# Performance work log

Hardware: AMD Instinct MI355X
Metric: run time of the kernel (lower is better)

## Reference

```python
import jax, jax.numpy as jnp
import numpy as np

DIM = 1280
HEADS = 16
HD = DIM // HEADS  # 80
NSEG = 8
LSEG = 1024
SEQ = NSEG * LSEG  # 8192


def _rotate_half(x):
    x1, x2 = jnp.split(x, 2, axis=-1)
    return jnp.concatenate([-x2, x1], axis=-1)


def setup_inputs() -> dict:
    key = jax.random.key(0)
    ks = jax.random.split(key, 6)
    hidden_states = jax.random.normal(ks[0], (SEQ, DIM), dtype=jnp.float32)
    # rotary embedding table: per-position angles over head_dim
    inv_freq = 1.0 / (10000.0 ** (np.arange(0, HD, 2, dtype=np.float32) / HD))
    pos = np.arange(SEQ, dtype=np.float32)
    freqs = np.outer(pos, inv_freq)                    # [SEQ, HD/2]
    emb = np.concatenate([freqs, freqs], axis=-1)      # [SEQ, HD]
    cos = jnp.asarray(np.cos(emb), dtype=jnp.float32)
    sin = jnp.asarray(np.sin(emb), dtype=jnp.float32)
    w_scale = 1.0 / np.sqrt(DIM)
    qkv_w = jax.random.normal(ks[1], (DIM, 3 * DIM), dtype=jnp.float32) * w_scale
    qkv_b = jax.random.normal(ks[2], (3 * DIM,), dtype=jnp.float32) * 0.02
    proj_w = jax.random.normal(ks[3], (DIM, DIM), dtype=jnp.float32) * w_scale
    proj_b = jax.random.normal(ks[4], (DIM,), dtype=jnp.float32) * 0.02
    cu_seqlens = jnp.arange(NSEG + 1, dtype=jnp.int32) * LSEG
    return {
        "hidden_states": hidden_states,
        "cos": cos,
        "sin": sin,
        "qkv_w": qkv_w,
        "qkv_b": qkv_b,
        "proj_w": proj_w,
        "proj_b": proj_b,
        "cu_seqlens": cu_seqlens,
    }


def reference(hidden_states, cos, sin, qkv_w, qkv_b, proj_w, proj_b, cu_seqlens):
    S, D = hidden_states.shape
    n_seg = cu_seqlens.shape[0] - 1          # static
    L = S // n_seg                            # equal-length packed segments
    # fused QKV projection: [S, 3D] -> q, k, v each [S, H, hd]
    qkv = hidden_states @ qkv_w + qkv_b
    q, k, v = (t.reshape(S, HEADS, HD) for t in jnp.split(qkv, 3, axis=-1))
    # RoPE (computed in fp32, as in apply_rotary_pos_emb_vision)
    c = cos.astype(jnp.float32)[:, None, :]   # [S, 1, hd]
    s = sin.astype(jnp.float32)[:, None, :]
    qf = q.astype(jnp.float32)
    kf = k.astype(jnp.float32)
    q = (qf * c + _rotate_half(qf) * s).astype(q.dtype)
    k = (kf * c + _rotate_half(kf) * s).astype(k.dtype)
    # block-diagonal varlen attention == independent attention per segment
    qs = q.reshape(n_seg, L, HEADS, HD)
    ks = k.reshape(n_seg, L, HEADS, HD)
    vs = v.reshape(n_seg, L, HEADS, HD)
    scale = HD ** -0.5
    scores = jnp.einsum("nqhd,nkhd->nhqk", qs, ks) * scale
    probs = jax.nn.softmax(scores.astype(jnp.float32), axis=-1).astype(qs.dtype)
    out = jnp.einsum("nhqk,nkhd->nqhd", probs, vs)     # [n, L, H, hd]
    out = out.reshape(S, D)
    return out @ proj_w + proj_b
```

## Files before the change

kernel.cpp:

```cpp
#include <hip/hip_runtime.h>

#define SEQ   8192
#define DIM   1280
#define HEADS 16
#define HD    80
#define LSEG  1024
#define QKVD  3840

typedef unsigned short USHORT;
typedef __attribute__((ext_vector_type(8))) short bf16x8;
typedef __attribute__((ext_vector_type(4))) float f32x4;
typedef __attribute__((ext_vector_type(4))) USHORT u16x4;
typedef __attribute__((ext_vector_type(4))) int i32x4;

#define CSF  0.16129832f

__device__ __forceinline__ USHORT f2bf(float x) {
  unsigned u = __float_as_uint(x);
  u += 0x7fffu + ((u >> 16) & 1u);
  return (USHORT)(u >> 16);
}
__device__ __forceinline__ float bf2f(USHORT b) {
  return __uint_as_float(((unsigned)b) << 16);
}
__device__ __forceinline__ void gload16(const void* g, void* l) {
  __builtin_amdgcn_global_load_lds(
      (const __attribute__((address_space(1))) void*)g,
      (__attribute__((address_space(3))) void*)l, 16, 0, 0);
}
__device__ __forceinline__ unsigned cvtpk(float a, float b) {
  unsigned d;
  asm("v_cvt_pk_bf16_f32 %0, %1, %2" : "=v"(d) : "v"(a), "v"(b));
  return d;
}
#define SB() __builtin_amdgcn_sched_barrier(0)

__global__ __launch_bounds__(256) void prep1(
    const float* __restrict__ hs, USHORT* __restrict__ hsB,
    const float* __restrict__ qkv_w, USHORT* __restrict__ qkvwT,
    const float* __restrict__ proj_w, USHORT* __restrict__ pwT) {
  __shared__ float tb[32][33];
  const int bx = blockIdx.x;
  const int tid = threadIdx.x;
  if (bx < 10240) {
    const int i = bx * 256 + tid;
    const float4 v = reinterpret_cast<const float4*>(hs)[i];
    USHORT* o = hsB + (size_t)i * 4;
    o[0] = f2bf(v.x); o[1] = f2bf(v.y); o[2] = f2bf(v.z); o[3] = f2bf(v.w);
    return;
  }
  const float* W; USHORT* T; int K, N, n0, k0;
  if (bx < 15040) {
    const int b = bx - 10240;
    W = qkv_w; T = qkvwT; K = DIM; N = QKVD;
    n0 = (b % 120) * 32; k0 = (b / 120) * 32;
  } else {
    const int b = bx - 15040;
    W = proj_w; T = pwT; K = DIM; N = DIM;
    n0 = (b % 40) * 32; k0 = (b / 40) * 32;
  }
  const int c = tid & 31, r0 = tid >> 5;
  for (int r = r0; r < 32; r += 8) tb[r][c] = W[(size_t)(k0 + r) * N + n0 + c];
  __syncthreads();
  for (int r = r0; r < 32; r += 8)
    T[(size_t)(n0 + r) * K + k0 + c] = f2bf(tb[c][r]);
}

__global__ __launch_bounds__(256) void prep2(
    USHORT* __restrict__ qkv, const float* __restrict__ cosb,
    const float* __restrict__ sinb, uint4* __restrict__ zb) {
  const int bx = blockIdx.x;
  const int tid = threadIdx.x;
  if (bx < 10240) {
    int idx = bx * 256 + tid;
    const int d4 = (idx % 10) * 4;
    int t = idx / 10;
    const int h = t % HEADS;
    t /= HEADS;
    const int qk = t & 1;
    const int s = t >> 1;
    USHORT* base = qkv + (size_t)s * QKVD + qk * DIM + h * HD;
    const u16x4 x1 = *(const u16x4*)&base[d4];
    const u16x4 x2 = *(const u16x4*)&base[d4 + 40];
    const f32x4 c1 = *(const f32x4*)&cosb[s * HD + d4];
    const f32x4 s1 = *(const f32x4*)&sinb[s * HD + d4];
    const f32x4 c2 = *(const f32x4*)&cosb[s * HD + d4 + 40];
    const f32x4 s2 = *(const f32x4*)&sinb[s * HD + d4 + 40];
    u16x4 o1, o2;
#pragma unroll
    for (int j = 0; j < 4; ++j) {
      const float a = bf2f(x1[j]), b = bf2f(x2[j]);
      o1[j] = f2bf(a * c1[j] - b * s1[j]);
      o2[j] = f2bf(b * c2[j] + a * s2[j]);
    }
    *(u16x4*)&base[d4] = o1;
    *(u16x4*)&base[d4 + 40] = o2;
    return;
  }
  if (tid < 64) zb[tid] = uint4{0u, 0u, 0u, 0u};
}

__global__ __launch_bounds__(512, 2) void mfma_gemm256(
    const USHORT* __restrict__ Ah, const USHORT* __restrict__ Bh,
    const float* __restrict__ bias, USHORT* __restrict__ Cout,
    USHORT* __restrict__ VtGo, int M, int N, int K, int lda) {
  extern __shared__ USHORT sm[];

  const int tid = threadIdx.x;
  const int l = tid & 63;
  const int w = tid >> 6;
  const int fr = l & 15;
  const int g = l >> 4;
  const int nrow = M >> 8;
  const int nwg = nrow * (N >> 8);
  const int orig = blockIdx.x;
  const int wg = (orig & 7) * (nwg >> 3) + (orig >> 3);
  const int row0 = (wg % nrow) << 8;
  const int col0 = (wg / nrow) << 8;
  const int wr = (w >> 2) << 7;
  const int wc = (w & 3) << 6;

  const f32x4 fz = {0.f, 0.f, 0.f, 0.f};
  f32x4 acc[8][4];
#pragma unroll
  for (int m = 0; m < 8; ++m)
#pragma unroll
    for (int n = 0; n < 4; ++n) acc[m][n] = fz;

  const int NT = K >> 6;

  const USHORT* asrc[4];
  const USHORT* bsrc[4];
#pragma unroll
  for (int i = 0; i < 4; ++i) {
    const int u = i * 512 + tid;
    const int row = u >> 3;
    const int c = (u & 7) ^ (row & 7);
    asrc[i] = Ah + (size_t)(row0 + row) * lda + c * 8;
    bsrc[i] = Bh + (size_t)(col0 + row) * K + c * 8;
  }
  auto stage = [&](int b) {
#pragma unroll
    for (int i = 0; i < 4; ++i) {
      USHORT* dst = sm + (i * 512 + (w << 6)) * 8 + b * 16384;
      gload16(asrc[i], dst);
      gload16(bsrc[i], dst + 32768);
    }
  };
  auto advance = [&]() {
#pragma unroll
    for (int i = 0; i < 4; ++i) { asrc[i] += 64; bsrc[i] += 64; }
  };

  const int fb = fr & 7;
  int aOff[2], bOff[2];
#pragma unroll
  for (int ks = 0; ks < 2; ++ks) {
    const int sl = (((ks << 2) + g) ^ fb) << 3;
    aOff[ks] = (wr + fr) * 64 + sl;
    bOff[ks] = 32768 + (wc + fr) * 64 + sl;
  }

  stage(0); advance();
  stage(1); advance();

  for (int t = 0; t < NT; ++t) {
    const int cur = t & 1;
    asm volatile("s_waitcnt vmcnt(8)" ::: "memory");
    SB();
    __builtin_amdgcn_s_barrier();
    SB();
    const int cb = cur << 14;
    bf16x8 ah[2][8], bh[2][4];
#pragma unroll
    for (int m = 0; m < 8; ++m)
      ah[0][m] = *(const bf16x8*)(sm + cb + aOff[0] + m * 1024);
#pragma unroll
    for (int n = 0; n < 4; ++n)
      bh[0][n] = *(const bf16x8*)(sm + cb + bOff[0] + n * 1024);
    SB();
#pragma unroll
    for (int m = 0; m < 8; ++m)
      ah[1][m] = *(const bf16x8*)(sm + cb + aOff[1] + m * 1024);
#pragma unroll
    for (int n = 0; n < 4; ++n)
      bh[1][n] = *(const bf16x8*)(sm + cb + bOff[1] + n * 1024);
    SB();
    asm volatile("s_waitcnt lgkmcnt(12)" ::: "memory");
    SB();
    __builtin_amdgcn_s_setprio(1);
#pragma unroll
    for (int m = 0; m < 8; ++m)
#pragma unroll
      for (int n = 0; n < 4; ++n)
        acc[m][n] = __builtin_amdgcn_mfma_f32_16x16x32_bf16(
            ah[0][m], bh[0][n], acc[m][n], 0, 0, 0);
    __builtin_amdgcn_s_setprio(0);
    SB();
    asm volatile("s_waitcnt lgkmcnt(0)" ::: "memory");
    SB();
    __builtin_amdgcn_s_barrier();
    SB();
    stage(cur);
    if (t < NT - 3) advance();
    SB();
    __builtin_amdgcn_s_setprio(1);
#pragma unroll
    for (int m = 0; m < 8; ++m)
#pragma unroll
      for (int n = 0; n < 4; ++n)
        acc[m][n] = __builtin_amdgcn_mfma_f32_16x16x32_bf16(
            ah[1][m], bh[1][n], acc[m][n], 0, 0, 0);
    __builtin_amdgcn_s_setprio(0);
  }

  asm volatile("s_waitcnt vmcnt(0)" ::: "memory");

  float bv[4];
#pragma unroll
  for (int n = 0; n < 4; ++n) bv[n] = bias[col0 + wc + n * 16 + fr];
#pragma unroll
  for (int m = 0; m < 8; ++m)
#pragma unroll
    for (int n = 0; n < 4; ++n) {
      const int colb = col0 + wc + n * 16;
      const int row = row0 + wr + m * 16 + g * 4;
      if (colb >= 2 * DIM) {
        u16x4 o;
#pragma unroll
        for (int r = 0; r < 4; ++r) o[r] = f2bf(acc[m][n][r] + bv[n]);
        const int rl = row & 63;
        const int sc = (rl & 0x23) | ((rl & 0x10) >> 2) | ((rl & 0x0C) << 1);
        *(u16x4*)&VtGo[(size_t)(colb + fr - 2 * DIM) * SEQ + (row & ~63) + sc] = o;
      } else {
#pragma unroll
        for (int r = 0; r < 4; ++r)
          Cout[(size_t)(row + r) * N + colb + fr] = f2bf(acc[m][n][r] + bv[n]);
      }
    }
}

__global__ __launch_bounds__(256) void mfma_gemm(
    const USHORT* __restrict__ Ah, const USHORT* __restrict__ Bh,
    const float* __restrict__ bias, float* __restrict__ Cout,
    int M, int N, int K, int lda) {
  __shared__ __align__(16) USHORT AhL[2][8192];
  __shared__ __align__(16) USHORT BhL[2][8192];

  const int tid = threadIdx.x;
  const int l = tid & 63;
  const int w = tid >> 6;
  const int nrow = M >> 7;
  const int nwg = nrow * (N >> 7);
  const int orig = blockIdx.x;
  const int wg = (orig & 7) * (nwg >> 3) + (orig >> 3);
  const int row0 = (wg % nrow) << 7;
  const int col0 = (wg / nrow) << 7;
  const int wr = (w >> 1) << 6;
  const int wc = (w & 1) << 6;

  const f32x4 fz = {0.f, 0.f, 0.f, 0.f};
  f32x4 acc[4][4];
#pragma unroll
  for (int m = 0; m < 4; ++m)
#pragma unroll
    for (int n = 0; n < 4; ++n) acc[m][n] = fz;

  const int fr = l & 15;
  const int g = l >> 4;
  const int NT = K >> 6;

  const USHORT* asrc[4];
  const USHORT* bsrc[4];
#pragma unroll
  for (int i = 0; i < 4; ++i) {
    const int u = (w * 4 + i) * 64 + l;
    const int row = u >> 3;
    const int c = (u & 7) ^ (row & 7);
    asrc[i] = Ah + (size_t)(row0 + row) * lda + c * 8;
    bsrc[i] = Bh + (size_t)(col0 + row) * K + c * 8;
  }
  auto stage = [&](int b) {
#pragma unroll
    for (int i = 0; i < 4; ++i) {
      gload16(asrc[i], &AhL[b][(w * 4 + i) * 512]);
      gload16(bsrc[i], &BhL[b][(w * 4 + i) * 512]);
    }
  };
  auto advance = [&]() {
#pragma unroll
    for (int i = 0; i < 4; ++i) { asrc[i] += 64; bsrc[i] += 64; }
  };

  const int fb = fr & 7;
  int aOff[2], bOff[2];
#pragma unroll
  for (int ks = 0; ks < 2; ++ks) {
    const int sl = (((ks << 2) + g) ^ fb) << 3;
    aOff[ks] = (wr + fr) * 64 + sl;
    bOff[ks] = (wc + fr) * 64 + sl;
  }
  const USHORT* AB = &AhL[0][0];
  const USHORT* BB = &BhL[0][0];

  stage(0); advance();
  stage(1); advance();

  for (int t = 0; t < NT; ++t) {
    const int cur = t & 1;
    asm volatile("s_waitcnt vmcnt(8)" ::: "memory");
    SB();
    __builtin_amdgcn_s_barrier();
    SB();
    const int cb = cur << 13;
    bf16x8 ah[2][4], bh[2][4];
#pragma unroll
    for (int m = 0; m < 4; ++m) {
      ah[0][m] = *(const bf16x8*)(AB + cb + aOff[0] + m * 1024);
      bh[0][m] = *(const bf16x8*)(BB + cb + bOff[0] + m * 1024);
    }
    SB();
#pragma unroll
    for (int m = 0; m < 4; ++m) {
      ah[1][m] = *(const bf16x8*)(AB + cb + aOff[1] + m * 1024);
      bh[1][m] = *(const bf16x8*)(BB + cb + bOff[1] + m * 1024);
    }
    SB();
    asm volatile("s_waitcnt lgkmcnt(8)" ::: "memory");
    SB();
    __builtin_amdgcn_s_setprio(1);
#pragma unroll
    for (int m = 0; m < 4; ++m)
#pragma unroll
      for (int n = 0; n < 4; ++n)
        acc[m][n] = __builtin_amdgcn_mfma_f32_16x16x32_bf16(
            ah[0][m], bh[0][n], acc[m][n], 0, 0, 0);
    __builtin_amdgcn_s_setprio(0);
    SB();
    asm volatile("s_waitcnt lgkmcnt(0)" ::: "memory");
    SB();
    __builtin_amdgcn_s_barrier();
    SB();
    stage(cur);
    if (t < NT - 3) advance();
    SB();
    __builtin_amdgcn_s_setprio(1);
#pragma unroll
    for (int m = 0; m < 4; ++m)
#pragma unroll
      for (int n = 0; n < 4; ++n)
        acc[m][n] = __builtin_amdgcn_mfma_f32_16x16x32_bf16(
            ah[1][m], bh[1][n], acc[m][n], 0, 0, 0);
    __builtin_amdgcn_s_setprio(0);
  }

  asm volatile("s_waitcnt vmcnt(0)" ::: "memory");

  float bv[4];
#pragma unroll
  for (int n = 0; n < 4; ++n) bv[n] = bias[col0 + wc + n * 16 + fr];
#pragma unroll
  for (int m = 0; m < 4; ++m)
#pragma unroll
    for (int n = 0; n < 4; ++n)
#pragma unroll
      for (int r = 0; r < 4; ++r) {
        const float v = acc[m][n][r] + bv[n];
        const int row = row0 + wr + m * 16 + (l >> 4) * 4 + r;
        const int col = col0 + wc + n * 16 + fr;
        Cout[(size_t)row * N + col] = v;
      }
}

__global__ __launch_bounds__(256, 3) void attn_mfma9(
    const USHORT* __restrict__ qkv, const USHORT* __restrict__ VtG,
    const USHORT* __restrict__ zbuf, USHORT* __restrict__ aoB) {
  const int h = blockIdx.y;
  const int bx = blockIdx.x;
  const int qb = (bx & 7) * 8 + (bx >> 3);
  const int s0 = qb * 128;
  const int k0g = (s0 / LSEG) * LSEG;
  const int tid = threadIdx.x;
  const int w = tid >> 6, l = tid & 63;
  const int g = l >> 4, fr = l & 15;
  const int q0 = s0 + w * 32;

  __shared__ __align__(16) USHORT Kl[2][64 * 128];
  __shared__ __align__(16) USHORT Vl[2][80 * 64];

  bf16x8 qb_frag[2][3];
#pragma unroll
  for (int nt2 = 0; nt2 < 2; ++nt2)
#pragma unroll
    for (int ks = 0; ks < 3; ++ks)
      qb_frag[nt2][ks] = *(const bf16x8*)
          &qkv[(size_t)(q0 + nt2 * 16 + fr) * QKVD + h * HD + ks * 32 + g * 8];

  const f32x4 fz = {0.f, 0.f, 0.f, 0.f};
  f32x4 oacc[2][5];
#pragma unroll
  for (int m = 0; m < 2; ++m)
#pragma unroll
    for (int n = 0; n < 5; ++n) oacc[m][n] = fz;
  float l_run[2] = {0.f, 0.f};

  const int nV = (w < 2) ? 3 : 2;
  const int vbase = (w < 2) ? w * 3 : 6 + (w - 2) * 2;
  const USHORT* ksrc[4];
  int kstep[4];
#pragma unroll
  for (int i = 0; i < 4; ++i) {
    const int t = (w * 4 + i) * 64 + l;
    const int row = t >> 4, c = (t & 15) ^ (row & 7);
    if (c < 10) {
      ksrc[i] = qkv + (size_t)(k0g + row) * QKVD + DIM + h * HD + c * 8;
      kstep[i] = 64 * QKVD;
    } else {
      ksrc[i] = zbuf;
      kstep[i] = 0;
    }
  }
  const USHORT* vsrc[3] = {zbuf, zbuf, zbuf};
#pragma unroll
  for (int i = 0; i < 3; ++i)
    if (i < nV) {
      const int u = (vbase + i) * 64 + l;
      const int row = u >> 3, c = (u & 7) ^ (row & 7);
      vsrc[i] = VtG + (size_t)(h * HD + row) * SEQ + k0g + c * 8;
    }

  auto stageKV = [&](int kb, int b) {
#pragma unroll
    for (int i = 0; i < 4; ++i)
      gload16(ksrc[i] + (size_t)kb * kstep[i], &Kl[b][(w * 4 + i) * 512]);
#pragma unroll
    for (int i = 0; i < 3; ++i)
      if (i < nV)
        gload16(vsrc[i] + kb * 64, &Vl[b][(vbase + i) * 512]);
  };

  const int fb = fr & 7;
  int kOff[3], vOff[2];
#pragma unroll
  for (int ks = 0; ks < 3; ++ks)
    kOff[ks] = fr * 128 + ((((ks << 2) + g) ^ fb) << 3);
#pragma unroll
  for (int ks = 0; ks < 2; ++ks)
    vOff[ks] = fr * 64 + ((((ks << 2) + g) ^ fb) << 3);
  const USHORT* KB = &Kl[0][0];
  const USHORT* VB = &Vl[0][0];

  stageKV(0, 0);
  stageKV(1, 1);

  for (int kb = 0; kb < 16; ++kb) {
    const int cur = kb & 1;
    if (w < 2) {
      asm volatile("s_waitcnt vmcnt(7)" ::: "memory");
    } else {
      asm volatile("s_waitcnt vmcnt(6)" ::: "memory");
    }
    SB();
    __builtin_amdgcn_s_barrier();
    SB();
    const int kcb = cur << 13;
    const int vcb = cur * 5120;

    f32x4 sc[4][2];
#pragma unroll
    for (int m = 0; m < 4; ++m)
#pragma unroll
      for (int nt2 = 0; nt2 < 2; ++nt2) sc[m][nt2] = fz;
    __builtin_amdgcn_s_setprio(1);
#pragma unroll
    for (int ks = 0; ks < 3; ++ks)
#pragma unroll
      for (int m = 0; m < 4; ++m) {
        const bf16x8 kbf = *(const bf16x8*)(KB + kcb + kOff[ks] + m * 2048);
#pragma unroll
        for (int nt2 = 0; nt2 < 2; ++nt2)
          sc[m][nt2] = __builtin_amdgcn_mfma_f32_16x16x32_bf16(
              kbf, qb_frag[nt2][ks], sc[m][nt2], 0, 0, 0);
      }
    __builtin_amdgcn_s_setprio(0);

    unsigned pkr[2][4][2];
#pragma unroll
    for (int nt2 = 0; nt2 < 2; ++nt2) {
      float ps = 0.f;
#pragma unroll
      for (int m = 0; m < 4; ++m) {
        float p[4];
#pragma unroll
        for (int j = 0; j < 4; ++j) {
          p[j] = exp2f(sc[m][nt2][j] * CSF);
          ps += p[j];
        }
        pkr[nt2][m][0] = cvtpk(p[0], p[1]);
        pkr[nt2][m][1] = cvtpk(p[2], p[3]);
      }
      ps += __shfl_xor(ps, 16);
      ps += __shfl_xor(ps, 32);
      l_run[nt2] += ps;
    }

#pragma unroll
    for (int ks = 0; ks < 2; ++ks) {
      union { bf16x8 v8; i32x4 i4; } pa[2];
#pragma unroll
      for (int mt2 = 0; mt2 < 2; ++mt2) {
        pa[mt2].i4[0] = (int)pkr[mt2][2 * ks][0];
        pa[mt2].i4[1] = (int)pkr[mt2][2 * ks][1];
        pa[mt2].i4[2] = (int)pkr[mt2][2 * ks + 1][0];
        pa[mt2].i4[3] = (int)pkr[mt2][2 * ks + 1][1];
      }
      __builtin_amdgcn_s_setprio(1);
#pragma unroll
      for (int nt = 0; nt < 5; ++nt) {
        const bf16x8 vb = *(const bf16x8*)(VB + vcb + vOff[ks] + nt * 1024);
#pragma unroll
        for (int mt2 = 0; mt2 < 2; ++mt2)
          oacc[mt2][nt] = __builtin_amdgcn_mfma_f32_16x16x32_bf16(
              pa[mt2].v8, vb, oacc[mt2][nt], 0, 0, 0);
      }
      __builtin_amdgcn_s_setprio(0);
    }

    __builtin_amdgcn_s_barrier();
    SB();
    const int kn = (kb + 2 < 16) ? kb + 2 : kb;
    stageKV(kn, cur);
    SB();
  }

  asm volatile("s_waitcnt vmcnt(0)" ::: "memory");

  float linv[2][4];
#pragma unroll
  for (int mt2 = 0; mt2 < 2; ++mt2)
#pragma unroll
    for (int j = 0; j < 4; ++j)
      linv[mt2][j] = 1.f / __shfl(l_run[mt2], 20 * g + j);
#pragma unroll
  for (int mt2 = 0; mt2 < 2; ++mt2)
#pragma unroll
    for (int nt = 0; nt < 5; ++nt)
#pragma unroll
      for (int j = 0; j < 4; ++j) {
        const int row = s0 + w * 32 + mt2 * 16 + g * 4 + j;
        const int col = h * HD + nt * 16 + fr;
        aoB[(size_t)row * QKVD + col] = f2bf(oacc[mt2][nt][j] * linv[mt2][j]);
      }
}

extern "C" void kernel_launch(void* const* d_in, const int* in_sizes, int n_in,
                              void* d_out, int out_size, void* d_ws,
                              size_t ws_size, hipStream_t stream) {
  const float* hs = (const float*)d_in[0];
  const float* cosb = (const float*)d_in[1];
  const float* sinb = (const float*)d_in[2];
  const float* qkv_w = (const float*)d_in[3];
  const float* qkv_b = (const float*)d_in[4];
  const float* proj_w = (const float*)d_in[5];
  const float* proj_b = (const float*)d_in[6];
  char* ws = (char*)d_ws;

  USHORT* qkvB  = (USHORT*)(ws);
  USHORT* hsB   = (USHORT*)(ws + 62914560u);
  USHORT* qkvwT = (USHORT*)(ws + 83886080u);
  USHORT* pwT   = (USHORT*)(ws + 93716480u);
  USHORT* VtG   = (USHORT*)d_out;
  USHORT* zbuf  = qkvwT;
  USHORT* aoB   = qkvB + 2 * DIM;

  hipFuncSetAttribute((const void*)mfma_gemm256,
                      hipFuncAttributeMaxDynamicSharedMemorySize, 131072);

  prep1<<<16640, 256, 0, stream>>>(hs, hsB, qkv_w, qkvwT, proj_w, pwT);
  mfma_gemm256<<<(SEQ / 256) * (QKVD / 256), 512, 131072, stream>>>(
      hsB, qkvwT, qkv_b, qkvB, VtG, SEQ, QKVD, DIM, DIM);
  prep2<<<10241, 256, 0, stream>>>(qkvB, cosb, sinb, (uint4*)zbuf);
  attn_mfma9<<<dim3(SEQ / 128, HEADS), 256, 0, stream>>>(qkvB, VtG, zbuf, aoB);
  mfma_gemm<<<(SEQ / 128) * (DIM / 128), 256, 0, stream>>>(
      aoB, pwT, proj_b, (float*)d_out, SEQ, DIM, DIM, QKVD);
}
```

Baseline: 254.4 us.

## Shrink QKV GEMM tile to 256x128 with triple-buffered LDS pipeline

The QKV projection GEMM changes from 256x256 output tiles with double buffering to 256x128 tiles with three LDS stages. The next global prefetch is issued right after the fragment reads, so there is one barrier per K-step instead of two. This doubles the number of workgroups so the grid fills the GPU better, and hides more load latency. In exchange, each tile reuses less data, the kernel uses more LDS (144 KB) and runs at occupancy 1, and per-wave accumulators shrink.

```diff
diff --git a/kernel.cpp b/kernel.cpp
--- a/kernel.cpp
+++ b/kernel.cpp
@@ -100,7 +100,7 @@
   if (tid < 64) zb[tid] = uint4{0u, 0u, 0u, 0u};
 }
 
-__global__ __launch_bounds__(512, 2) void mfma_gemm256(
+__global__ __launch_bounds__(512, 1) void mfma_gemm256(
     const USHORT* __restrict__ Ah, const USHORT* __restrict__ Bh,
     const float* __restrict__ bias, USHORT* __restrict__ Cout,
     USHORT* __restrict__ VtGo, int M, int N, int K, int lda) {
@@ -112,44 +112,52 @@
   const int fr = l & 15;
   const int g = l >> 4;
   const int nrow = M >> 8;
-  const int nwg = nrow * (N >> 8);
+  const int nwg = nrow * (N >> 7);
   const int orig = blockIdx.x;
   const int wg = (orig & 7) * (nwg >> 3) + (orig >> 3);
   const int row0 = (wg % nrow) << 8;
-  const int col0 = (wg / nrow) << 8;
-  const int wr = (w >> 2) << 7;
-  const int wc = (w & 3) << 6;
+  const int col0 = (wg / nrow) << 7;
+  const int wr = (w >> 1) << 6;
+  const int wc = (w & 1) << 6;
 
   const f32x4 fz = {0.f, 0.f, 0.f, 0.f};
-  f32x4 acc[8][4];
-#pragma unroll
-  for (int m = 0; m < 8; ++m)
+  f32x4 acc[4][4];
+#pragma unroll
+  for (int m = 0; m < 4; ++m)
 #pragma unroll
     for (int n = 0; n < 4; ++n) acc[m][n] = fz;
 
   const int NT = K >> 6;
 
   const USHORT* asrc[4];
-  const USHORT* bsrc[4];
+  const USHORT* bsrc[2];
 #pragma unroll
   for (int i = 0; i < 4; ++i) {
     const int u = i * 512 + tid;
     const int row = u >> 3;
     const int c = (u & 7) ^ (row & 7);
     asrc[i] = Ah + (size_t)(row0 + row) * lda + c * 8;
+  }
+#pragma unroll
+  for (int i = 0; i < 2; ++i) {
+    const int u = i * 512 + tid;
+    const int row = u >> 3;
+    const int c = (u & 7) ^ (row & 7);
     bsrc[i] = Bh + (size_t)(col0 + row) * K + c * 8;
   }
   auto stage = [&](int b) {
 #pragma unroll
-    for (int i = 0; i < 4; ++i) {
-      USHORT* dst = sm + (i * 512 + (w << 6)) * 8 + b * 16384;
-      gload16(asrc[i], dst);
-      gload16(bsrc[i], dst + 32768);
-    }
+    for (int i = 0; i < 4; ++i)
+      gload16(asrc[i], sm + b * 16384 + (i * 512 + (w << 6)) * 8);
+#pragma unroll
+    for (int i = 0; i < 2; ++i)
+      gload16(bsrc[i], sm + 49152 + b * 8192 + (i * 512 + (w << 6)) * 8);
   };
   auto advance = [&]() {
 #pragma unroll
-    for (int i = 0; i < 4; ++i) { asrc[i] += 64; bsrc[i] += 64; }
+    for (int i = 0; i < 4; ++i) asrc[i] += 64;
+#pragma unroll
+    for (int i = 0; i < 2; ++i) bsrc[i] += 64;
   };
 
   const int fb = fr & 7;
@@ -158,60 +166,44 @@
   for (int ks = 0; ks < 2; ++ks) {
     const int sl = (((ks << 2) + g) ^ fb) << 3;
     aOff[ks] = (wr + fr) * 64 + sl;
-    bOff[ks] = 32768 + (wc + fr) * 64 + sl;
+    bOff[ks] = 49152 + (wc + fr) * 64 + sl;
   }
 
   stage(0); advance();
   stage(1); advance();
 
+  int cur = 0, sb = 2;
   for (int t = 0; t < NT; ++t) {
-    const int cur = t & 1;
-    asm volatile("s_waitcnt vmcnt(8)" ::: "memory");
+    asm volatile("s_waitcnt vmcnt(6)" ::: "memory");
     SB();
     __builtin_amdgcn_s_barrier();
     SB();
-    const int cb = cur << 14;
-    bf16x8 ah[2][8], bh[2][4];
-#pragma unroll
-    for (int m = 0; m < 8; ++m)
-      ah[0][m] = *(const bf16x8*)(sm + cb + aOff[0] + m * 1024);
-#pragma unroll
-    for (int n = 0; n < 4; ++n)
-      bh[0][n] = *(const bf16x8*)(sm + cb + bOff[0] + n * 1024);
-    SB();
-#pragma unroll
-    for (int m = 0; m < 8; ++m)
-      ah[1][m] = *(const bf16x8*)(sm + cb + aOff[1] + m * 1024);
-#pragma unroll
-    for (int n = 0; n < 4; ++n)
-      bh[1][n] = *(const bf16x8*)(sm + cb + bOff[1] + n * 1024);
-    SB();
-    asm volatile("s_waitcnt lgkmcnt(12)" ::: "memory");
+    const int ca = cur * 16384, cbb = cur * 8192;
+    bf16x8 ah[2][4], bh[2][4];
+#pragma unroll
+    for (int ks = 0; ks < 2; ++ks)
+#pragma unroll
+      for (int m = 0; m < 4; ++m) {
+        ah[ks][m] = *(const bf16x8*)(sm + ca + aOff[ks] + m * 1024);
+        bh[ks][m] = *(const bf16x8*)(sm + cbb + bOff[ks] + m * 1024);
+      }
+    stage(sb);
+    if (t < NT - 3) advance();
+    SB();
+    asm volatile("s_waitcnt lgkmcnt(0)" ::: "memory");
     SB();
     __builtin_amdgcn_s_setprio(1);
 #pragma unroll
-    for (int m = 0; m < 8; ++m)
-#pragma unroll
-      for (int n = 0; n < 4; ++n)
-        acc[m][n] = __builtin_amdgcn_mfma_f32_16x16x32_bf16(
-            ah[0][m], bh[0][n], acc[m][n], 0, 0, 0);
+    for (int ks = 0; ks < 2; ++ks)
+#pragma unroll
+      for (int m = 0; m < 4; ++m)
+#pragma unroll
+        for (int n = 0; n < 4; ++n)
+          acc[m][n] = __builtin_amdgcn_mfma_f32_16x16x32_bf16(
+              ah[ks][m], bh[ks][n], acc[m][n], 0, 0, 0);
     __builtin_amdgcn_s_setprio(0);
-    SB();
-    asm volatile("s_waitcnt lgkmcnt(0)" ::: "memory");
-    SB();
-    __builtin_amdgcn_s_barrier();
-    SB();
-    stage(cur);
-    if (t < NT - 3) advance();
-    SB();
-    __builtin_amdgcn_s_setprio(1);
-#pragma unroll
-    for (int m = 0; m < 8; ++m)
-#pragma unroll
-      for (int n = 0; n < 4; ++n)
-        acc[m][n] = __builtin_amdgcn_mfma_f32_16x16x32_bf16(
-            ah[1][m], bh[1][n], acc[m][n], 0, 0, 0);
-    __builtin_amdgcn_s_setprio(0);
+    cur = (cur == 2) ? 0 : cur + 1;
+    sb = (sb == 2) ? 0 : sb + 1;
   }
 
   asm volatile("s_waitcnt vmcnt(0)" ::: "memory");
@@ -220,7 +212,7 @@
 #pragma unroll
   for (int n = 0; n < 4; ++n) bv[n] = bias[col0 + wc + n * 16 + fr];
 #pragma unroll
-  for (int m = 0; m < 8; ++m)
+  for (int m = 0; m < 4; ++m)
 #pragma unroll
     for (int n = 0; n < 4; ++n) {
       const int colb = col0 + wc + n * 16;
@@ -574,10 +566,10 @@
   USHORT* aoB   = qkvB + 2 * DIM;
 
   hipFuncSetAttribute((const void*)mfma_gemm256,
-                      hipFuncAttributeMaxDynamicSharedMemorySize, 131072);
+                      hipFuncAttributeMaxDynamicSharedMemorySize, 147456);
 
   prep1<<<16640, 256, 0, stream>>>(hs, hsB, qkv_w, qkvwT, proj_w, pwT);
-  mfma_gemm256<<<(SEQ / 256) * (QKVD / 256), 512, 131072, stream>>>(
+  mfma_gemm256<<<(SEQ / 256) * (QKVD / 128), 512, 147456, stream>>>(
       hsB, qkvwT, qkv_b, qkvB, VtG, SEQ, QKVD, DIM, DIM);
   prep2<<<10241, 256, 0, stream>>>(qkvB, cosb, sinb, (uint4*)zbuf);
   attn_mfma9<<<dim3(SEQ / 128, HEADS), 256, 0, stream>>>(qkvB, VtG, zbuf, aoB);
```

After: 304.6 us. 19.7% more time.

## Split QKV GEMM main loop into four smaller LDS-load/MFMA phases

Applied to the files above, without the earlier changes.

Restructures the QKV GEMM inner loop so that operand fragments come from LDS in four smaller phases (half of the A rows at a time), each followed by a full lgkmcnt wait, 16 MFMAs and a workgroup barrier, instead of loading all fragments up front. The aim is to cut register pressure from holding 24 bf16x8 fragments, which could raise occupancy or avoid spills. The cost is extra barriers and full LDS waits, which serialise LDS loads with MFMA work and remove the overlap the old lgkmcnt(12) partial wait gave. Global staging for the next tile now starts only after all four phases, so load/compute overlap within an iteration shrinks.

```diff
diff --git a/kernel.cpp b/kernel.cpp
--- a/kernel.cpp
+++ b/kernel.cpp
@@ -171,47 +171,88 @@
     __builtin_amdgcn_s_barrier();
     SB();
     const int cb = cur << 14;
-    bf16x8 ah[2][8], bh[2][4];
-#pragma unroll
-    for (int m = 0; m < 8; ++m)
-      ah[0][m] = *(const bf16x8*)(sm + cb + aOff[0] + m * 1024);
+    bf16x8 a0[4], a1[4], bh[4];
+
+#pragma unroll
+    for (int m = 0; m < 4; ++m)
+      a0[m] = *(const bf16x8*)(sm + cb + aOff[0] + m * 1024);
 #pragma unroll
     for (int n = 0; n < 4; ++n)
-      bh[0][n] = *(const bf16x8*)(sm + cb + bOff[0] + n * 1024);
-    SB();
-#pragma unroll
-    for (int m = 0; m < 8; ++m)
-      ah[1][m] = *(const bf16x8*)(sm + cb + aOff[1] + m * 1024);
-#pragma unroll
-    for (int n = 0; n < 4; ++n)
-      bh[1][n] = *(const bf16x8*)(sm + cb + bOff[1] + n * 1024);
-    SB();
-    asm volatile("s_waitcnt lgkmcnt(12)" ::: "memory");
+      bh[n] = *(const bf16x8*)(sm + cb + bOff[0] + n * 1024);
+    SB();
+    asm volatile("s_waitcnt lgkmcnt(0)" ::: "memory");
     SB();
     __builtin_amdgcn_s_setprio(1);
 #pragma unroll
-    for (int m = 0; m < 8; ++m)
+    for (int m = 0; m < 4; ++m)
 #pragma unroll
       for (int n = 0; n < 4; ++n)
         acc[m][n] = __builtin_amdgcn_mfma_f32_16x16x32_bf16(
-            ah[0][m], bh[0][n], acc[m][n], 0, 0, 0);
+            a0[m], bh[n], acc[m][n], 0, 0, 0);
     __builtin_amdgcn_s_setprio(0);
     SB();
+    __builtin_amdgcn_s_barrier();
+    SB();
+
+#pragma unroll
+    for (int m = 0; m < 4; ++m)
+      a1[m] = *(const bf16x8*)(sm + cb + aOff[0] + (m + 4) * 1024);
+    SB();
     asm volatile("s_waitcnt lgkmcnt(0)" ::: "memory");
+    SB();
+    __builtin_amdgcn_s_setprio(1);
+#pragma unroll
+    for (int m = 0; m < 4; ++m)
+#pragma unroll
+      for (int n = 0; n < 4; ++n)
+        acc[m + 4][n] = __builtin_amdgcn_mfma_f32_16x16x32_bf16(
+            a1[m], bh[n], acc[m + 4][n], 0, 0, 0);
+    __builtin_amdgcn_s_setprio(0);
+    SB();
+    __builtin_amdgcn_s_barrier();
+    SB();
+
+#pragma unroll
+    for (int m = 0; m < 4; ++m)
+      a0[m] = *(const bf16x8*)(sm + cb + aOff[1] + m * 1024);
+#pragma unroll
+    for (int n = 0; n < 4; ++n)
+      bh[n] = *(const bf16x8*)(sm + cb + bOff[1] + n * 1024);
+    SB();
+    asm volatile("s_waitcnt lgkmcnt(0)" ::: "memory");
+    SB();
+    __builtin_amdgcn_s_setprio(1);
+#pragma unroll
+    for (int m = 0; m < 4; ++m)
+#pragma unroll
+      for (int n = 0; n < 4; ++n)
+        acc[m][n] = __builtin_amdgcn_mfma_f32_16x16x32_bf16(
+            a0[m], bh[n], acc[m][n], 0, 0, 0);
+    __builtin_amdgcn_s_setprio(0);
+    SB();
+    __builtin_amdgcn_s_barrier();
+    SB();
+
+#pragma unroll
+    for (int m = 0; m < 4; ++m)
+      a1[m] = *(const bf16x8*)(sm + cb + aOff[1] + (m + 4) * 1024);
+    SB();
+    asm volatile("s_waitcnt lgkmcnt(0)" ::: "memory");
+    SB();
+    __builtin_amdgcn_s_setprio(1);
+#pragma unroll
+    for (int m = 0; m < 4; ++m)
+#pragma unroll
+      for (int n = 0; n < 4; ++n)
+        acc[m + 4][n] = __builtin_amdgcn_mfma_f32_16x16x32_bf16(
+            a1[m], bh[n], acc[m + 4][n], 0, 0, 0);
+    __builtin_amdgcn_s_setprio(0);
     SB();
     __builtin_amdgcn_s_barrier();
     SB();
     stage(cur);
     if (t < NT - 3) advance();
     SB();
-    __builtin_amdgcn_s_setprio(1);
-#pragma unroll
-    for (int m = 0; m < 8; ++m)
-#pragma unroll
-      for (int n = 0; n < 4; ++n)
-        acc[m][n] = __builtin_amdgcn_mfma_f32_16x16x32_bf16(
-            ah[1][m], bh[1][n], acc[m][n], 0, 0, 0);
-    __builtin_amdgcn_s_setprio(0);
   }
 
   asm volatile("s_waitcnt vmcnt(0)" ::: "memory");
```

Measured after the change: 262.4 us. +3.1%, slower.
